# Performance work log

Measured on AMD Instinct MI355X. Metric: run time of the kernel, lower is better.

The kernel has to match this reference:

```python
import jax, jax.numpy as jnp
import numpy as np

TOP_K = 8
NUM_EXPERTS = 256
NUM_GROUPS = 8
TOPK_GROUP = 4
SCALE = 2.5
EPS = 1e-20


def setup_inputs() -> dict:
    key = jax.random.key(0)
    k1, k2, k3 = jax.random.split(key, 3)
    T, H = 8192, 7168
    hidden_states = jax.random.normal(k1, (T, H), dtype=jnp.float32)
    # scale ~ kaiming-ish so logits are O(1) and sigmoid is not saturated
    weight = jax.random.normal(k2, (NUM_EXPERTS, H), dtype=jnp.float32) * (H ** -0.5)
    e_score_correction_bias = jax.random.normal(k3, (NUM_EXPERTS,), dtype=jnp.float32) * 0.1
    return {"hidden_states": hidden_states, "weight": weight,
            "e_score_correction_bias": e_score_correction_bias}


def reference(hidden_states, weight, e_score_correction_bias):
    T = hidden_states.shape[0]
    epg = NUM_EXPERTS // NUM_GROUPS  # experts per group
    # gating logits: [T, E]
    logits = jnp.einsum('th,eh->te', hidden_states.astype(jnp.float32),
                        weight.astype(jnp.float32))
    scores = jax.nn.sigmoid(logits)
    scores_for_choice = scores + e_score_correction_bias[None, :]
    # group score = sum of top-2 corrected scores within each group: [T, G]
    grouped = scores_for_choice.reshape(T, NUM_GROUPS, epg)
    top2, _ = jax.lax.top_k(grouped, 2)
    group_scores = top2.sum(axis=-1)
    # select topk_group groups, build mask [T, G]
    _, group_idx = jax.lax.top_k(group_scores, TOPK_GROUP)
    group_mask = jnp.zeros((T, NUM_GROUPS), dtype=scores.dtype)
    group_mask = group_mask.at[jnp.arange(T)[:, None], group_idx].set(1.0)
    # expand to expert mask [T, E]
    score_mask = jnp.repeat(group_mask, epg, axis=1)
    tmp_scores = jnp.where(score_mask > 0, scores_for_choice, 0.0)
    # top_k experts among allowed groups
    _, topk_idx = jax.lax.top_k(tmp_scores, TOP_K)
    # gather UNcorrected scores as weights
    topk_weight = jnp.take_along_axis(scores, topk_idx, axis=1)
    topk_weight = topk_weight / (topk_weight.sum(axis=-1, keepdims=True) + EPS)
    topk_weight = topk_weight * SCALE
    return topk_idx, topk_weight
```

## Files before the change

### kernel.cpp

```cpp
#include <hip/hip_runtime.h>
#include <cmath>

typedef __attribute__((ext_vector_type(8))) _Float16 half8;
typedef __attribute__((ext_vector_type(4))) float f32x4;

#define HH 7168
#define NE 256
#define NQ 224
#define NITER 56
#define TOPK 8
#define TOPKG 4

#define C1 (1.f/2048.f)
#define C2 (1.f/4194304.f)

__device__ __forceinline__ void split3(float x, unsigned short& h, unsigned short& m, unsigned short& l){
  const _Float16 hh = (_Float16)x;
  const float r1 = x - (float)hh;
  const _Float16 mm = (_Float16)(r1 * 2048.f);
  const float r2 = r1 - (float)mm * C1;
  const _Float16 ll = (_Float16)(r2 * 4194304.f);
  h = __builtin_bit_cast(unsigned short, hh);
  m = __builtin_bit_cast(unsigned short, mm);
  l = __builtin_bit_cast(unsigned short, ll);
}

__global__ __launch_bounds__(256) void prep_w(const float* __restrict__ wgt,
                                              unsigned short* __restrict__ bh,
                                              unsigned short* __restrict__ bm,
                                              unsigned short* __restrict__ bl){
  const int g = blockIdx.x*256 + threadIdx.x;
  const int e = g / (HH/4);
  const int k0 = (g - e*(HH/4))*4;
  const float4 wv = *(const float4*)(wgt + (size_t)e*HH + k0);
  const float v[4] = {wv.x, wv.y, wv.z, wv.w};
  unsigned short h4[4], m4[4], l4[4];
#pragma unroll
  for(int i=0;i<4;i++) split3(v[i], h4[i], m4[i], l4[i]);
  const int q = k0>>5, lq = (k0>>3)&3, j0 = k0&7;
  const int nt = e>>4, n16 = e&15;
  const int L = lq*16 + n16;
  const size_t base = ((size_t)(q*16+nt)*64 + L)*8 + j0;
  *(ushort4*)(bh+base) = make_ushort4(h4[0],h4[1],h4[2],h4[3]);
  *(ushort4*)(bm+base) = make_ushort4(m4[0],m4[1],m4[2],m4[3]);
  *(ushort4*)(bl+base) = make_ushort4(l4[0],l4[1],l4[2],l4[3]);
}

__device__ __forceinline__ void stageA(unsigned short* alds, int buf, int tok, int k0, const float4* ga){
#pragma unroll
  for(int u=0;u<4;u++){
    const float vv[4] = {ga[u].x, ga[u].y, ga[u].z, ga[u].w};
    unsigned short h4[4], m4[4], l4[4];
#pragma unroll
    for(int p=0;p<4;p++) split3(vv[p], h4[p], m4[p], l4[p]);
    const int ui = tok*136 + k0 + 4*u;
    *(ushort4*)&alds[(buf*3+0)*4352 + ui] = make_ushort4(h4[0],h4[1],h4[2],h4[3]);
    *(ushort4*)&alds[(buf*3+1)*4352 + ui] = make_ushort4(m4[0],m4[1],m4[2],m4[3]);
    *(ushort4*)&alds[(buf*3+2)*4352 + ui] = make_ushort4(l4[0],l4[1],l4[2],l4[3]);
  }
}

__global__ __launch_bounds__(256,1)
void moe_gate(const float* __restrict__ hs,
              const unsigned short* __restrict__ bhp,
              const unsigned short* __restrict__ bmp,
              const unsigned short* __restrict__ blp,
              const float* __restrict__ bias,
              float* __restrict__ out, int T){
  __shared__ __align__(16) unsigned char smem[52224];
  unsigned short* alds = (unsigned short*)smem;
  float (*sfc)[NE] = (float (*)[NE])smem;

  const int tid = threadIdx.x, lane = tid&63, w = tid>>6;
  const int tb = blockIdx.x*32;

  const half8* __restrict__ bhv = (const half8*)bhp;
  const half8* __restrict__ bmv = (const half8*)bmp;
  const half8* __restrict__ blv = (const half8*)blp;

  float biasv[4];
#pragma unroll
  for(int nt=0;nt<4;nt++) biasv[nt] = bias[w*64 + nt*16 + (lane&15)];

  f32x4 ksum[2][4], kcmp[2][4];
#pragma unroll
  for(int mt=0;mt<2;mt++)
#pragma unroll
    for(int nt=0;nt<4;nt++){ ksum[mt][nt] = f32x4{0,0,0,0}; kcmp[mt][nt] = f32x4{0,0,0,0}; }

  const int tokS = tid>>3, k0S = (tid&7)*16;
  const float* agp = hs + (size_t)(tb+tokS)*HH + k0S;

  {
    float4 ga[4];
#pragma unroll
    for(int u=0;u<4;u++) ga[u] = *(const float4*)(agp + 4*u);
    stageA(alds, 0, tokS, k0S, ga);
  }
  half8 Bh[4], Bm[4], Bl[4];
#pragma unroll
  for(int nt=0;nt<4;nt++){
    const int slot = (w*4 + nt)*64 + lane;
    Bh[nt] = bhv[slot]; Bm[nt] = bmv[slot]; Bl[nt] = blv[slot];
  }
  __syncthreads();

  for(int i=0;i<NITER;i++){
    const int cur = i&1, nb = cur^1;
    float4 ga[4];
    if(i+1<NITER){
      const float* ap = agp + (size_t)(i+1)*128;
#pragma unroll
      for(int u=0;u<4;u++) ga[u] = *(const float4*)(ap + 4*u);
    }
    f32x4 a0[2][4], a1[2][4], a2[2][4];
#pragma unroll
    for(int mt=0;mt<2;mt++)
#pragma unroll
      for(int nt=0;nt<4;nt++){ a0[mt][nt]=f32x4{0,0,0,0}; a1[mt][nt]=f32x4{0,0,0,0}; a2[mt][nt]=f32x4{0,0,0,0}; }

#pragma unroll
    for(int s=0;s<4;s++){
      const int q = i*4+s;
      half8 ah[2], am[2], al[2];
#pragma unroll
      for(int mt=0;mt<2;mt++){
        const int off = (mt*16 + (lane&15))*136 + 32*s + 8*(lane>>4);
        ah[mt] = *(const half8*)&alds[(cur*3+0)*4352 + off];
        am[mt] = *(const half8*)&alds[(cur*3+1)*4352 + off];
        al[mt] = *(const half8*)&alds[(cur*3+2)*4352 + off];
      }
      half8 BhN[4], BmN[4], BlN[4];
      const bool more = (q+1 < NQ);
      if(more){
#pragma unroll
        for(int nt=0;nt<4;nt++){
          const int slot = ((q+1)*16 + w*4 + nt)*64 + lane;
          BhN[nt] = bhv[slot]; BmN[nt] = bmv[slot]; BlN[nt] = blv[slot];
        }
      }
#pragma unroll
      for(int mt=0;mt<2;mt++)
#pragma unroll
        for(int nt=0;nt<4;nt++){
          a0[mt][nt] = __builtin_amdgcn_mfma_f32_16x16x32_f16(ah[mt], Bh[nt], a0[mt][nt], 0,0,0);
          a1[mt][nt] = __builtin_amdgcn_mfma_f32_16x16x32_f16(ah[mt], Bm[nt], a1[mt][nt], 0,0,0);
          a1[mt][nt] = __builtin_amdgcn_mfma_f32_16x16x32_f16(am[mt], Bh[nt], a1[mt][nt], 0,0,0);
          a2[mt][nt] = __builtin_amdgcn_mfma_f32_16x16x32_f16(ah[mt], Bl[nt], a2[mt][nt], 0,0,0);
          a2[mt][nt] = __builtin_amdgcn_mfma_f32_16x16x32_f16(al[mt], Bh[nt], a2[mt][nt], 0,0,0);
          a2[mt][nt] = __builtin_amdgcn_mfma_f32_16x16x32_f16(am[mt], Bm[nt], a2[mt][nt], 0,0,0);
        }
      if(more){
#pragma unroll
        for(int nt=0;nt<4;nt++){ Bh[nt]=BhN[nt]; Bm[nt]=BmN[nt]; Bl[nt]=BlN[nt]; }
      }
    }
    if(i+1<NITER) stageA(alds, nb, tokS, k0S, ga);
#pragma unroll
    for(int mt=0;mt<2;mt++)
#pragma unroll
      for(int nt=0;nt<4;nt++)
#pragma unroll
        for(int r=0;r<4;r++){
          const float v = a0[mt][nt][r] + a1[mt][nt][r]*C1 + a2[mt][nt][r]*C2;
          const float y = v - kcmp[mt][nt][r];
          const float t = ksum[mt][nt][r] + y;
          kcmp[mt][nt][r] = (t - ksum[mt][nt][r]) - y;
          ksum[mt][nt][r] = t;
        }
    __syncthreads();
  }

#pragma unroll
  for(int mt=0;mt<2;mt++)
#pragma unroll
    for(int nt=0;nt<4;nt++)
#pragma unroll
      for(int r=0;r<4;r++){
        const int tok = mt*16 + (lane>>4)*4 + r;
        const int e = w*64 + nt*16 + (lane&15);
        const float lg = ksum[mt][nt][r] - kcmp[mt][nt][r];
        const float sg = 1.f/(1.f + expf(-lg));
        sfc[tok][e] = sg + biasv[nt];
      }
  __syncthreads();

  const float4 bias4 = *(const float4*)(bias + 4*lane);
  const int g = lane >> 3;
  const float NEG_INF = -__builtin_inff();

  for (int it = 0; it < 8; ++it) {
    const int t = w * 8 + it;
    const float4 s4 = *(const float4*)&sfc[t][4*lane];

    float m1 = s4.x, m2 = NEG_INF;
    if (s4.y > m1) { m2 = m1; m1 = s4.y; } else if (s4.y > m2) m2 = s4.y;
    if (s4.z > m1) { m2 = m1; m1 = s4.z; } else if (s4.z > m2) m2 = s4.z;
    if (s4.w > m1) { m2 = m1; m1 = s4.w; } else if (s4.w > m2) m2 = s4.w;
#pragma unroll
    for (int m = 1; m <= 4; m <<= 1) {
      const float o1 = __shfl_xor(m1, m);
      const float o2 = __shfl_xor(m2, m);
      const float nm1 = fmaxf(m1, o1);
      const float nm2 = fmaxf(fminf(m1, o1), fmaxf(m2, o2));
      m1 = nm1; m2 = nm2;
    }
    const float gs = m1 + m2;

    float gsv[8];
#pragma unroll
    for (int j = 0; j < 8; ++j) gsv[j] = __shfl(gs, j * 8);

    unsigned gm = 0;
#pragma unroll
    for (int r = 0; r < TOPKG; ++r) {
      float best = NEG_INF; int bj = 0;
#pragma unroll
      for (int j = 0; j < 8; ++j) {
        const bool avail = !((gm >> j) & 1u);
        if (avail && gsv[j] > best) { best = gsv[j]; bj = j; }
      }
      gm |= 1u << bj;
    }
    const bool allowed = (gm >> g) & 1u;

    float v0 = allowed ? s4.x : 0.f;
    float v1 = allowed ? s4.y : 0.f;
    float v2 = allowed ? s4.z : 0.f;
    float v3 = allowed ? s4.w : 0.f;

    float sumw = 0.f;
    int myidx = 0; float myraw = 0.f;
#pragma unroll
    for (int r = 0; r < TOPK; ++r) {
      float bv = v0; int bj = 0;
      if (v1 > bv) { bv = v1; bj = 1; }
      if (v2 > bv) { bv = v2; bj = 2; }
      if (v3 > bv) { bv = v3; bj = 3; }
      int bidx = 4 * lane + bj;
#pragma unroll
      for (int m = 1; m < 64; m <<= 1) {
        const float ov = __shfl_xor(bv, m);
        const int   oi = __shfl_xor(bidx, m);
        if (ov > bv || (ov == bv && oi < bidx)) { bv = ov; bidx = oi; }
      }
      const int oj = bidx & 3;
      const float cand = (oj == 0) ? (s4.x - bias4.x)
                       : (oj == 1) ? (s4.y - bias4.y)
                       : (oj == 2) ? (s4.z - bias4.z)
                       :             (s4.w - bias4.w);
      const float raw = __shfl(cand, bidx >> 2);
      sumw += raw;
      if (lane == r) { myidx = bidx; myraw = raw; }
      if (lane == (bidx >> 2)) {
        if      (oj == 0) v0 = NEG_INF;
        else if (oj == 1) v1 = NEG_INF;
        else if (oj == 2) v2 = NEG_INF;
        else              v3 = NEG_INF;
      }
    }

    if (lane < TOPK) {
      const size_t gt = (size_t)(tb + t);
      out[gt * TOPK + lane] = (float)myidx;
      out[(size_t)T * TOPK + gt * TOPK + lane] = myraw / (sumw + 1e-20f) * 2.5f;
    }
  }
}

extern "C" void kernel_launch(void* const* d_in, const int* in_sizes, int n_in,
                              void* d_out, int out_size, void* d_ws, size_t ws_size,
                              hipStream_t stream) {
  const float* hs   = (const float*)d_in[0];
  const float* wgt  = (const float*)d_in[1];
  const float* bias = (const float*)d_in[2];
  float* out = (float*)d_out;

  const int T = in_sizes[0] / HH;

  unsigned short* bh = (unsigned short*)d_ws;
  unsigned short* bm = bh + (size_t)NE*HH;
  unsigned short* bl = bm + (size_t)NE*HH;

  hipLaunchKernelGGL(prep_w, dim3(NE*HH/4/256), dim3(256), 0, stream, wgt, bh, bm, bl);
  hipLaunchKernelGGL(moe_gate, dim3(T/32), dim3(256), 0, stream, hs, bh, bm, bl, bias, out, T);
}
```

Measured before the change: 551.0 us.

## Use two-level fp16 split with weight scaling and split GEMM from gating kernel

Drops the third fp16 split level so each k-step issues four MFMAs instead of six per tile, with weights scaled by 1024 to keep fp16 residuals representable. The fused kernel is split into a 512-thread GEMM kernel tiled 64 tokens by 128 experts, with a reorganised LDS layout, that writes logits to a workspace buffer. A separate gate kernel then does sigmoid and grouped top-k selection. This cuts matrix-core work but adds a global round trip for the logits and an extra launch, and the reduced split precision may change selection on near-ties.

```diff
diff --git a/kernel.cpp b/kernel.cpp
--- a/kernel.cpp
+++ b/kernel.cpp
@@ -2,6 +2,7 @@
 #include <cmath>
 
 typedef __attribute__((ext_vector_type(8))) _Float16 half8;
+typedef __attribute__((ext_vector_type(8))) unsigned short ushort8;
 typedef __attribute__((ext_vector_type(4))) float f32x4;
 
 #define HH 7168
@@ -10,188 +11,193 @@
 #define NITER 56
 #define TOPK 8
 #define TOPKG 4
-
+#define WSC 1024.f
+#define INV_WS (1.f/1024.f)
 #define C1 (1.f/2048.f)
 #define C2 (1.f/4194304.f)
 
-__device__ __forceinline__ void split3(float x, unsigned short& h, unsigned short& m, unsigned short& l){
+__device__ __forceinline__ void split2(float x, unsigned short& h, unsigned short& m){
   const _Float16 hh = (_Float16)x;
-  const float r1 = x - (float)hh;
-  const _Float16 mm = (_Float16)(r1 * 2048.f);
-  const float r2 = r1 - (float)mm * C1;
-  const _Float16 ll = (_Float16)(r2 * 4194304.f);
+  const float r = x - (float)hh;
+  const _Float16 mm = (_Float16)(r * 2048.f);
   h = __builtin_bit_cast(unsigned short, hh);
   m = __builtin_bit_cast(unsigned short, mm);
-  l = __builtin_bit_cast(unsigned short, ll);
 }
 
 __global__ __launch_bounds__(256) void prep_w(const float* __restrict__ wgt,
                                               unsigned short* __restrict__ bh,
-                                              unsigned short* __restrict__ bm,
-                                              unsigned short* __restrict__ bl){
-  const int g = blockIdx.x*256 + threadIdx.x;
-  const int e = g / (HH/4);
-  const int k0 = (g - e*(HH/4))*4;
-  const float4 wv = *(const float4*)(wgt + (size_t)e*HH + k0);
-  const float v[4] = {wv.x, wv.y, wv.z, wv.w};
-  unsigned short h4[4], m4[4], l4[4];
-#pragma unroll
-  for(int i=0;i<4;i++) split3(v[i], h4[i], m4[i], l4[i]);
-  const int q = k0>>5, lq = (k0>>3)&3, j0 = k0&7;
-  const int nt = e>>4, n16 = e&15;
-  const int L = lq*16 + n16;
-  const size_t base = ((size_t)(q*16+nt)*64 + L)*8 + j0;
-  *(ushort4*)(bh+base) = make_ushort4(h4[0],h4[1],h4[2],h4[3]);
-  *(ushort4*)(bm+base) = make_ushort4(m4[0],m4[1],m4[2],m4[3]);
-  *(ushort4*)(bl+base) = make_ushort4(l4[0],l4[1],l4[2],l4[3]);
-}
-
-__device__ __forceinline__ void stageA(unsigned short* alds, int buf, int tok, int k0, const float4* ga){
-#pragma unroll
-  for(int u=0;u<4;u++){
-    const float vv[4] = {ga[u].x, ga[u].y, ga[u].z, ga[u].w};
-    unsigned short h4[4], m4[4], l4[4];
-#pragma unroll
-    for(int p=0;p<4;p++) split3(vv[p], h4[p], m4[p], l4[p]);
-    const int ui = tok*136 + k0 + 4*u;
-    *(ushort4*)&alds[(buf*3+0)*4352 + ui] = make_ushort4(h4[0],h4[1],h4[2],h4[3]);
-    *(ushort4*)&alds[(buf*3+1)*4352 + ui] = make_ushort4(m4[0],m4[1],m4[2],m4[3]);
-    *(ushort4*)&alds[(buf*3+2)*4352 + ui] = make_ushort4(l4[0],l4[1],l4[2],l4[3]);
-  }
-}
-
-__global__ __launch_bounds__(256,1)
-void moe_gate(const float* __restrict__ hs,
-              const unsigned short* __restrict__ bhp,
-              const unsigned short* __restrict__ bmp,
-              const unsigned short* __restrict__ blp,
-              const float* __restrict__ bias,
-              float* __restrict__ out, int T){
-  __shared__ __align__(16) unsigned char smem[52224];
-  unsigned short* alds = (unsigned short*)smem;
-  float (*sfc)[NE] = (float (*)[NE])smem;
-
-  const int tid = threadIdx.x, lane = tid&63, w = tid>>6;
-  const int tb = blockIdx.x*32;
+                                              unsigned short* __restrict__ bm){
+  const int b = blockIdx.x;
+  const int nt = b & 15, qb = (b >> 4) * 4;
+  const int w = threadIdx.x >> 6, L = threadIdx.x & 63;
+  const int q = qb + w;
+  const int e = nt*16 + (L & 15);
+  const int k0 = 32*q + 8*(L >> 4);
+  const float4 a0 = *(const float4*)(wgt + (size_t)e*HH + k0);
+  const float4 a1 = *(const float4*)(wgt + (size_t)e*HH + k0 + 4);
+  const float v[8] = {a0.x,a0.y,a0.z,a0.w,a1.x,a1.y,a1.z,a1.w};
+  ushort8 h8, m8;
+#pragma unroll
+  for(int j=0;j<8;j++){ unsigned short hh,mm; split2(v[j]*WSC, hh, mm); h8[j]=hh; m8[j]=mm; }
+  const size_t base = ((size_t)(q*16+nt)*64 + L)*8;
+  *(ushort8*)(bh+base) = h8;
+  *(ushort8*)(bm+base) = m8;
+}
+
+#define STIDX(buf,lvl,mt,q,row) (((((buf)*2+(lvl))*16 + (mt)*4 + (q))*64 + (row))*8)
+__global__ __launch_bounds__(512,2)
+void gemm(const float* __restrict__ hs,
+          const unsigned short* __restrict__ bhp,
+          const unsigned short* __restrict__ bmp,
+          float* __restrict__ lgout){
+  __shared__ __align__(16) unsigned short alds[32768];
+
+  const int tid = threadIdx.x, lane = tid & 63, w = tid >> 6;
+  const int b = blockIdx.x;
+  const int slice = (b >> 2) & 1;
+  const int tg = (b >> 3)*4 + (b & 3);
+  const int tb = tg*64, eb = slice*128;
+  const int mtp = w >> 2, ntp = w & 3;
 
   const half8* __restrict__ bhv = (const half8*)bhp;
   const half8* __restrict__ bmv = (const half8*)bmp;
-  const half8* __restrict__ blv = (const half8*)blp;
-
-  float biasv[4];
-#pragma unroll
-  for(int nt=0;nt<4;nt++) biasv[nt] = bias[w*64 + nt*16 + (lane&15)];
-
-  f32x4 ksum[2][4], kcmp[2][4];
-#pragma unroll
-  for(int mt=0;mt<2;mt++)
-#pragma unroll
-    for(int nt=0;nt<4;nt++){ ksum[mt][nt] = f32x4{0,0,0,0}; kcmp[mt][nt] = f32x4{0,0,0,0}; }
-
-  const int tokS = tid>>3, k0S = (tid&7)*16;
-  const float* agp = hs + (size_t)(tb+tokS)*HH + k0S;
-
-  {
-    float4 ga[4];
-#pragma unroll
-    for(int u=0;u<4;u++) ga[u] = *(const float4*)(agp + 4*u);
-    stageA(alds, 0, tokS, k0S, ga);
-  }
-  half8 Bh[4], Bm[4], Bl[4];
-#pragma unroll
-  for(int nt=0;nt<4;nt++){
-    const int slot = (w*4 + nt)*64 + lane;
-    Bh[nt] = bhv[slot]; Bm[nt] = bmv[slot]; Bl[nt] = blv[slot];
+
+  f32x4 ksum[2][2], kcmp[2][2];
+#pragma unroll
+  for(int a=0;a<2;a++)
+#pragma unroll
+    for(int c=0;c<2;c++){ ksum[a][c]=f32x4{0,0,0,0}; kcmp[a][c]=f32x4{0,0,0,0}; }
+
+  const int tokS = tid >> 3, cS = tid & 7;
+  const int mtS = tokS >> 4, m16S = tokS & 15, qS = cS >> 1;
+  const int rowA = (cS & 1)*32 + m16S;
+  const float* agp = hs + (size_t)(tb + tokS)*HH + cS*16;
+
+  float4 ga[4];
+#pragma unroll
+  for(int u=0;u<4;u++) ga[u] = *(const float4*)(agp + 4*u);
+
+  auto stage = [&](int buf){
+    unsigned short h[16], m[16];
+    const float* gv = (const float*)ga;
+#pragma unroll
+    for(int p=0;p<16;p++) split2(gv[p], h[p], m[p]);
+#pragma unroll
+    for(int lvl=0; lvl<2; lvl++){
+      const unsigned short* src = lvl ? m : h;
+      ushort8 lo, hi;
+#pragma unroll
+      for(int j=0;j<8;j++){ lo[j]=src[j]; hi[j]=src[8+j]; }
+      const int ia = STIDX(buf,lvl,mtS,qS,rowA);
+      *(ushort8*)&alds[ia]        = lo;
+      *(ushort8*)&alds[ia + 128]  = hi;
+    }
+  };
+
+  stage(0);
+  half8 Bh[2], Bm[2];
+#pragma unroll
+  for(int ntl=0;ntl<2;ntl++){
+    const int slot = ((0*16 + slice*8 + ntp*2 + ntl)*64 + lane);
+    Bh[ntl] = bhv[slot]; Bm[ntl] = bmv[slot];
   }
   __syncthreads();
 
   for(int i=0;i<NITER;i++){
-    const int cur = i&1, nb = cur^1;
-    float4 ga[4];
-    if(i+1<NITER){
+    const int cur = i & 1, nb = cur ^ 1;
+    if(i+1 < NITER){
       const float* ap = agp + (size_t)(i+1)*128;
 #pragma unroll
       for(int u=0;u<4;u++) ga[u] = *(const float4*)(ap + 4*u);
     }
-    f32x4 a0[2][4], a1[2][4], a2[2][4];
-#pragma unroll
-    for(int mt=0;mt<2;mt++)
-#pragma unroll
-      for(int nt=0;nt<4;nt++){ a0[mt][nt]=f32x4{0,0,0,0}; a1[mt][nt]=f32x4{0,0,0,0}; a2[mt][nt]=f32x4{0,0,0,0}; }
+    f32x4 c0[2][2], c1[2][2], c2[2][2];
+#pragma unroll
+    for(int a=0;a<2;a++)
+#pragma unroll
+      for(int c=0;c<2;c++){ c0[a][c]=f32x4{0,0,0,0}; c1[a][c]=f32x4{0,0,0,0}; c2[a][c]=f32x4{0,0,0,0}; }
 
 #pragma unroll
     for(int s=0;s<4;s++){
-      const int q = i*4+s;
-      half8 ah[2], am[2], al[2];
-#pragma unroll
-      for(int mt=0;mt<2;mt++){
-        const int off = (mt*16 + (lane&15))*136 + 32*s + 8*(lane>>4);
-        ah[mt] = *(const half8*)&alds[(cur*3+0)*4352 + off];
-        am[mt] = *(const half8*)&alds[(cur*3+1)*4352 + off];
-        al[mt] = *(const half8*)&alds[(cur*3+2)*4352 + off];
-      }
-      half8 BhN[4], BmN[4], BlN[4];
+      const int q = i*4 + s;
+      half8 ah[2], am[2];
+#pragma unroll
+      for(int mtl=0;mtl<2;mtl++){
+        const int mt = mtp*2 + mtl;
+        ah[mtl] = *(const half8*)&alds[STIDX(cur,0,mt,s,lane)];
+        am[mtl] = *(const half8*)&alds[STIDX(cur,1,mt,s,lane)];
+      }
+      half8 BhN[2], BmN[2];
       const bool more = (q+1 < NQ);
       if(more){
 #pragma unroll
-        for(int nt=0;nt<4;nt++){
-          const int slot = ((q+1)*16 + w*4 + nt)*64 + lane;
-          BhN[nt] = bhv[slot]; BmN[nt] = bmv[slot]; BlN[nt] = blv[slot];
+        for(int ntl=0;ntl<2;ntl++){
+          const int slot = (((q+1)*16 + slice*8 + ntp*2 + ntl)*64 + lane);
+          BhN[ntl] = bhv[slot]; BmN[ntl] = bmv[slot];
         }
       }
 #pragma unroll
-      for(int mt=0;mt<2;mt++)
-#pragma unroll
-        for(int nt=0;nt<4;nt++){
-          a0[mt][nt] = __builtin_amdgcn_mfma_f32_16x16x32_f16(ah[mt], Bh[nt], a0[mt][nt], 0,0,0);
-          a1[mt][nt] = __builtin_amdgcn_mfma_f32_16x16x32_f16(ah[mt], Bm[nt], a1[mt][nt], 0,0,0);
-          a1[mt][nt] = __builtin_amdgcn_mfma_f32_16x16x32_f16(am[mt], Bh[nt], a1[mt][nt], 0,0,0);
-          a2[mt][nt] = __builtin_amdgcn_mfma_f32_16x16x32_f16(ah[mt], Bl[nt], a2[mt][nt], 0,0,0);
-          a2[mt][nt] = __builtin_amdgcn_mfma_f32_16x16x32_f16(al[mt], Bh[nt], a2[mt][nt], 0,0,0);
-          a2[mt][nt] = __builtin_amdgcn_mfma_f32_16x16x32_f16(am[mt], Bm[nt], a2[mt][nt], 0,0,0);
+      for(int mtl=0;mtl<2;mtl++)
+#pragma unroll
+        for(int ntl=0;ntl<2;ntl++){
+          c0[mtl][ntl] = __builtin_amdgcn_mfma_f32_16x16x32_f16(ah[mtl], Bh[ntl], c0[mtl][ntl], 0,0,0);
+          c1[mtl][ntl] = __builtin_amdgcn_mfma_f32_16x16x32_f16(ah[mtl], Bm[ntl], c1[mtl][ntl], 0,0,0);
+          c1[mtl][ntl] = __builtin_amdgcn_mfma_f32_16x16x32_f16(am[mtl], Bh[ntl], c1[mtl][ntl], 0,0,0);
+          c2[mtl][ntl] = __builtin_amdgcn_mfma_f32_16x16x32_f16(am[mtl], Bm[ntl], c2[mtl][ntl], 0,0,0);
         }
       if(more){
 #pragma unroll
-        for(int nt=0;nt<4;nt++){ Bh[nt]=BhN[nt]; Bm[nt]=BmN[nt]; Bl[nt]=BlN[nt]; }
-      }
-    }
-    if(i+1<NITER) stageA(alds, nb, tokS, k0S, ga);
-#pragma unroll
-    for(int mt=0;mt<2;mt++)
-#pragma unroll
-      for(int nt=0;nt<4;nt++)
+        for(int ntl=0;ntl<2;ntl++){ Bh[ntl]=BhN[ntl]; Bm[ntl]=BmN[ntl]; }
+      }
+    }
+    if(i+1 < NITER) stage(nb);
+#pragma unroll
+    for(int a=0;a<2;a++)
+#pragma unroll
+      for(int c=0;c<2;c++)
 #pragma unroll
         for(int r=0;r<4;r++){
-          const float v = a0[mt][nt][r] + a1[mt][nt][r]*C1 + a2[mt][nt][r]*C2;
-          const float y = v - kcmp[mt][nt][r];
-          const float t = ksum[mt][nt][r] + y;
-          kcmp[mt][nt][r] = (t - ksum[mt][nt][r]) - y;
-          ksum[mt][nt][r] = t;
+          const float v = c0[a][c][r] + c1[a][c][r]*C1 + c2[a][c][r]*C2;
+          const float y = v - kcmp[a][c][r];
+          const float t = ksum[a][c][r] + y;
+          kcmp[a][c][r] = (t - ksum[a][c][r]) - y;
+          ksum[a][c][r] = t;
         }
     __syncthreads();
   }
 
 #pragma unroll
-  for(int mt=0;mt<2;mt++)
-#pragma unroll
-    for(int nt=0;nt<4;nt++)
+  for(int mtl=0;mtl<2;mtl++)
+#pragma unroll
+    for(int ntl=0;ntl<2;ntl++)
 #pragma unroll
       for(int r=0;r<4;r++){
-        const int tok = mt*16 + (lane>>4)*4 + r;
-        const int e = w*64 + nt*16 + (lane&15);
-        const float lg = ksum[mt][nt][r] - kcmp[mt][nt][r];
-        const float sg = 1.f/(1.f + expf(-lg));
-        sfc[tok][e] = sg + biasv[nt];
-      }
-  __syncthreads();
-
+        const int tok = (mtp*2+mtl)*16 + (lane>>4)*4 + r;
+        const int e = (ntp*2+ntl)*16 + (lane&15);
+        const float lg = (ksum[mtl][ntl][r] - kcmp[mtl][ntl][r]) * INV_WS;
+        lgout[(size_t)(tb+tok)*NE + eb + e] = lg;
+      }
+}
+
+__global__ __launch_bounds__(256)
+void gate(const float* __restrict__ lg, const float* __restrict__ bias,
+          float* __restrict__ out, int T){
+  const int tid = threadIdx.x, lane = tid & 63, wv = tid >> 6;
+  const int tb = blockIdx.x*32;
   const float4 bias4 = *(const float4*)(bias + 4*lane);
   const int g = lane >> 3;
   const float NEG_INF = -__builtin_inff();
 
   for (int it = 0; it < 8; ++it) {
-    const int t = w * 8 + it;
-    const float4 s4 = *(const float4*)&sfc[t][4*lane];
+    const int t = tb + wv*8 + it;
+    const float4 l4 = *(const float4*)(lg + (size_t)t*NE + 4*lane);
+    float4 r4;
+    r4.x = 1.f/(1.f + expf(-l4.x));
+    r4.y = 1.f/(1.f + expf(-l4.y));
+    r4.z = 1.f/(1.f + expf(-l4.z));
+    r4.w = 1.f/(1.f + expf(-l4.w));
+    float4 s4;
+    s4.x = r4.x + bias4.x; s4.y = r4.y + bias4.y;
+    s4.z = r4.z + bias4.z; s4.w = r4.w + bias4.w;
 
     float m1 = s4.x, m2 = NEG_INF;
     if (s4.y > m1) { m2 = m1; m1 = s4.y; } else if (s4.y > m2) m2 = s4.y;
@@ -245,10 +251,10 @@
         if (ov > bv || (ov == bv && oi < bidx)) { bv = ov; bidx = oi; }
       }
       const int oj = bidx & 3;
-      const float cand = (oj == 0) ? (s4.x - bias4.x)
-                       : (oj == 1) ? (s4.y - bias4.y)
-                       : (oj == 2) ? (s4.z - bias4.z)
-                       :             (s4.w - bias4.w);
+      const float cand = (oj == 0) ? r4.x
+                       : (oj == 1) ? r4.y
+                       : (oj == 2) ? r4.z
+                       :             r4.w;
       const float raw = __shfl(cand, bidx >> 2);
       sumw += raw;
       if (lane == r) { myidx = bidx; myraw = raw; }
@@ -261,9 +267,8 @@
     }
 
     if (lane < TOPK) {
-      const size_t gt = (size_t)(tb + t);
-      out[gt * TOPK + lane] = (float)myidx;
-      out[(size_t)T * TOPK + gt * TOPK + lane] = myraw / (sumw + 1e-20f) * 2.5f;
+      out[(size_t)t * TOPK + lane] = (float)myidx;
+      out[(size_t)T * TOPK + (size_t)t * TOPK + lane] = myraw / (sumw + 1e-20f) * 2.5f;
     }
   }
 }
@@ -280,8 +285,9 @@
 
   unsigned short* bh = (unsigned short*)d_ws;
   unsigned short* bm = bh + (size_t)NE*HH;
-  unsigned short* bl = bm + (size_t)NE*HH;
-
-  hipLaunchKernelGGL(prep_w, dim3(NE*HH/4/256), dim3(256), 0, stream, wgt, bh, bm, bl);
-  hipLaunchKernelGGL(moe_gate, dim3(T/32), dim3(256), 0, stream, hs, bh, bm, bl, bias, out, T);
-}
+  float* lgbuf = (float*)(bm + (size_t)NE*HH);
+
+  hipLaunchKernelGGL(prep_w, dim3(896), dim3(256), 0, stream, wgt, bh, bm);
+  hipLaunchKernelGGL(gemm,   dim3(256), dim3(512), 0, stream, hs, bh, bm, lgbuf);
+  hipLaunchKernelGGL(gate,   dim3(T/32), dim3(256), 0, stream, lgbuf, bias, out, T);
+}
```

Measured after the change: 499.5 us. -9.4%, faster.
